# Kernel tuning notes

Measured on AMD Instinct MI355X. Metric: run time of the kernel, lower is better.

The kernel has to match this reference:

```python
import jax, jax.numpy as jnp
import numpy as np

N, E, DIM, L, NPERM, B = 20000, 640000, 128, 4, 20000, 256
R = NPERM * L * L  # rows of perm matrices
EPS = 1e-5


def _mlp(x, w1, b1, g, beta, w2, b2):
    # Linear -> BatchNorm (training-mode batch stats) -> ReLU -> Linear
    h = x @ w1 + b1
    mu = h.mean(0)
    var = h.var(0)  # biased, matches torch BN normalization
    h = (h - mu) * jax.lax.rsqrt(var + EPS) * g + beta
    return jax.nn.relu(h) @ w2 + b2


def setup_inputs() -> dict:
    key = jax.random.key(0)
    ks = jax.random.split(key, 40)
    s = 0.05
    inp = {}
    inp["node_feat"] = jax.random.normal(ks[0], (N, DIM), jnp.float32)
    inp["edge_feat"] = jax.random.normal(ks[1], (E, DIM), jnp.float32)
    inp["src"] = jax.random.randint(ks[2], (E,), 0, N)
    inp["dst"] = jax.random.randint(ks[3], (E,), 0, N)
    inp["rev_flag"] = jax.random.randint(ks[4], (E,), 0, 2).astype(bool)
    # sparse node_to_perm / edge_to_perm: one nnz per row (row i implicit)
    inp["n2p_cols"] = jax.random.randint(ks[5], (R,), 0, N)
    inp["n2p_vals"] = jax.random.uniform(ks[6], (R,), jnp.float32)
    inp["e2p_cols"] = jax.random.randint(ks[7], (R,), 0, E)
    inp["e2p_vals"] = jax.random.uniform(ks[8], (R,), jnp.float32)
    # sparse pooling matrix: perm j -> graph pool_rows[j] with weight pool_vals[j]
    inp["pool_rows"] = jax.random.randint(ks[9], (NPERM,), 0, B)
    inp["pool_vals"] = jax.random.uniform(ks[10], (NPERM,), jnp.float32)
    for i, n in enumerate(["in_w", "out_w", "src_w", "dst_w", "nloop_w", "eloop_w"]):
        inp[n] = jax.random.normal(ks[11 + i], (DIM, DIM), jnp.float32) * s
    inp["lrp_w"] = jax.random.normal(ks[17], (DIM, DIM, L * L), jnp.float32) * s
    inp["nbias"] = jnp.zeros((DIM,), jnp.float32)
    inp["ebias"] = jnp.zeros((DIM,), jnp.float32)
    inp["lrp_bias"] = jnp.zeros((DIM,), jnp.float32)
    for p, k0 in (("n", 20), ("e", 26)):
        inp[p + "mlp_w1"] = jax.random.normal(ks[k0], (DIM, DIM), jnp.float32) * s
        inp[p + "mlp_b1"] = jnp.zeros((DIM,), jnp.float32)
        inp[p + "mlp_g"] = jnp.ones((DIM,), jnp.float32)
        inp[p + "mlp_beta"] = jnp.zeros((DIM,), jnp.float32)
        inp[p + "mlp_w2"] = jax.random.normal(ks[k0 + 1], (DIM, DIM), jnp.float32) * s
        inp[p + "mlp_b2"] = jnp.zeros((DIM,), jnp.float32)
    return inp


def reference(node_feat, edge_feat, src, dst, rev_flag, n2p_cols, n2p_vals,
              e2p_cols, e2p_vals, pool_rows, pool_vals,
              in_w, out_w, src_w, dst_w, nloop_w, eloop_w, lrp_w,
              nbias, ebias, lrp_bias,
              nmlp_w1, nmlp_b1, nmlp_g, nmlp_beta, nmlp_w2, nmlp_b2,
              emlp_w1, emlp_b1, emlp_g, emlp_beta, emlp_w2, emlp_b2):
    hs = node_feat[src]   # [E, d]
    hd = node_feat[dst]   # [E, d]
    r = rev_flag[:, None]
    # per-edge messages with reverse-edge masking
    edge_msg = jnp.where(r, hs @ dst_w - hd @ src_w, hd @ dst_w - hs @ src_w)
    node_msg = jnp.where(r, edge_feat @ out_w, -(edge_feat @ in_w))
    node_agg = jax.ops.segment_sum(node_msg, dst, num_segments=N)
    # node update
    nout = _mlp(node_feat @ nloop_w + node_agg + nbias,
                nmlp_w1, nmlp_b1, nmlp_g, nmlp_beta, nmlp_w2, nmlp_b2)
    # edge update: degree-scaled term uses out-degree of dst node
    out_deg = jax.ops.segment_sum(jnp.ones((E,), jnp.float32), src, num_segments=N)
    dlog = jnp.log2(1.0 + out_deg[dst])[:, None]
    add = 2.0 * (1.0 + dlog) * (edge_feat @ (src_w - dst_w))
    eout = _mlp(edge_feat @ eloop_w + add + edge_msg + ebias,
                emlp_w1, emlp_b1, emlp_g, emlp_beta, emlp_w2, emlp_b2)
    # sparse perm gathers + LRP einsum + sparse pooling scatter
    perm = n2p_vals[:, None] * nout[n2p_cols] + e2p_vals[:, None] * eout[e2p_cols]
    perm = perm.reshape(NPERM, L * L, DIM)
    lrp = jnp.einsum('dab,bca->dc', perm, lrp_w) + lrp_bias
    pooled = jax.ops.segment_sum(pool_vals[:, None] * lrp, pool_rows, num_segments=B)
    return pooled, eout
```

## Files before the change

kernel.cpp:

```cpp
#include <hip/hip_runtime.h>
#include <stdint.h>

constexpr int Nn     = 20000;
constexpr int Ee     = 640000;
constexpr int NPERMc = 20000;

using bf16x8 = __attribute__((ext_vector_type(8))) short;
using f32x4  = __attribute__((ext_vector_type(4))) float;
using s16x4  = __attribute__((ext_vector_type(4))) short;
using u16x8  = __attribute__((ext_vector_type(8))) unsigned short;

__device__ __forceinline__ short f2bf(float f) {
  union { float f; unsigned u; } v; v.f = f;
  unsigned r = v.u + 0x7FFFu + ((v.u >> 16) & 1u);
  return (short)(r >> 16);
}
__device__ __forceinline__ float bf2f(unsigned short s) {
  union { unsigned u; float f; } v; v.u = ((unsigned)s) << 16;
  return v.f;
}
__device__ __forceinline__ f32x4 MFMA(bf16x8 a, bf16x8 b, f32x4 c) {
  return __builtin_amdgcn_mfma_f32_16x16x32_bf16(a, b, c, 0, 0, 0);
}

__device__ __forceinline__ int fragIdx(int k, int n) {
  int t = n >> 4, kk = k >> 5;
  int l = ((k & 31) >> 3) * 16 + (n & 15);
  int j = k & 7;
  return ((t * 4 + kk) * 64 + l) * 8 + j;
}

__device__ __forceinline__ void stage16x128(const float* __restrict__ src, int row0, int M,
                                            int lane, short* lds) {
  #pragma unroll
  for (int it = 0; it < 8; ++it) {
    int u = it * 64 + lane;
    int r = u >> 5;
    int q = u & 31;
    int row = row0 + r;
    float4 v = make_float4(0.f, 0.f, 0.f, 0.f);
    if (row < M) v = ((const float4*)(src + (size_t)row * 128))[q];
    int k  = q * 4;
    int kk = k >> 5;
    int l2 = ((k & 31) >> 3) * 16 + r;
    int j  = k & 7;
    s16x4 s4 = { f2bf(v.x), f2bf(v.y), f2bf(v.z), f2bf(v.w) };
    *(s16x4*)(lds + (kk * 64 + l2) * 8 + j) = s4;
  }
}

__global__ __launch_bounds__(256) void kPrep(
    const float* __restrict__ in_w,  const float* __restrict__ out_w,
    const float* __restrict__ src_w, const float* __restrict__ dst_w,
    const float* __restrict__ nloop_w, const float* __restrict__ eloop_w,
    const float* __restrict__ lrp_w,
    const float* __restrict__ nbias, const float* __restrict__ ebias,
    const float* __restrict__ w1e, const float* __restrict__ b1e,
    const float* __restrict__ w1n, const float* __restrict__ b1n,
    const float* __restrict__ w2e, const float* __restrict__ w2n,
    short* __restrict__ WA, short* __restrict__ BQ, short* __restrict__ WN,
    short* __restrict__ W2E, short* __restrict__ W2N, short* __restrict__ WL,
    float* __restrict__ c0e, float* __restrict__ c0n) {
  __shared__ float Rl[16384];
  int tid = threadIdx.x;
  int blk = blockIdx.x;
  if (blk < 448) {
    int p = blk >> 6, sub = blk & 63;
    const float* La; const float* Lb = nullptr; const float* R; short* outp;
    float sOut = 1.f;
    switch (p) {
      case 0: La = eloop_w;             R = w1e; outp = WA;          break;
      case 1: La = src_w; Lb = dst_w;   R = w1e; outp = WA + 16384;  break;
      case 2: La = dst_w;               R = w1e; outp = BQ;          break;
      case 3: La = src_w;               R = w1e; outp = BQ + 16384;  break;
      case 4: La = nloop_w;             R = w1n; outp = WN;          break;
      case 5: La = out_w;               R = w1n; outp = WN + 16384;  break;
      default: La = in_w;               R = w1n; outp = WN + 32768; sOut = -1.f; break;
    }
    for (int i = tid; i < 16384; i += 256) Rl[i] = R[i];
    __syncthreads();
    int e = sub * 256 + tid;
    int k = e >> 7, n = e & 127;
    float acc = 0.f;
    bool hasLb = (Lb != nullptr);
    for (int j = 0; j < 128; ++j) {
      float l = La[k * 128 + j];
      if (hasLb) l -= Lb[k * 128 + j];
      acc += l * Rl[j * 128 + n];
    }
    outp[fragIdx(k, n)] = f2bf(acc * sOut);
  } else if (blk < 512) {
    int e = (blk - 448) * 256 + tid; int k = e >> 7, n = e & 127;
    W2E[fragIdx(k, n)] = f2bf(w2e[k * 128 + n]);
  } else if (blk < 576) {
    int e = (blk - 512) * 256 + tid; int k = e >> 7, n = e & 127;
    W2N[fragIdx(k, n)] = f2bf(w2n[k * 128 + n]);
  } else if (blk < 1600) {
    int q = blk - 576; int a = q >> 6;
    int e = (q & 63) * 256 + tid; int k = e >> 7, n = e & 127;
    WL[a * 16384 + fragIdx(k, n)] = f2bf(lrp_w[(k * 128 + n) * 16 + a]);
  } else {
    if (tid < 128) {
      float acc = 0.f;
      for (int k2 = 0; k2 < 128; ++k2) acc += ebias[k2] * w1e[k2 * 128 + tid];
      c0e[tid] = acc + b1e[tid];
    } else {
      int n = tid - 128; float acc = 0.f;
      for (int k2 = 0; k2 < 128; ++k2) acc += nbias[k2] * w1n[k2 * 128 + n];
      c0n[n] = acc + b1n[n];
    }
  }
}


__global__ __launch_bounds__(256) void kHist(
    const int* __restrict__ srcI, const int* __restrict__ dstI,
    int* __restrict__ cnt, float* __restrict__ deg) {
  int e = blockIdx.x * 256 + threadIdx.x;
  atomicAdd(&cnt[dstI[e]], 1);
  atomicAdd(&deg[srcI[e]], 1.0f);
}

__global__ __launch_bounds__(256) void kScan(const int* __restrict__ cnt,
                                             int* __restrict__ off,
                                             int* __restrict__ cur) {
  __shared__ int lc[Nn];
  __shared__ int ps[256];
  int tid = threadIdx.x;
  for (int i = tid; i < Nn; i += 256) lc[i] = cnt[i];
  __syncthreads();
  constexpr int CH = (Nn + 255) / 256;
  int base = tid * CH;
  int local = 0;
  for (int i = 0; i < CH; ++i) {
    int idx = base + i;
    if (idx < Nn) local += lc[idx];
  }
  ps[tid] = local;
  __syncthreads();
  for (int d = 1; d < 256; d <<= 1) {
    int t = (tid >= d) ? ps[tid - d] : 0;
    __syncthreads();
    if (tid >= d) ps[tid] += t;
    __syncthreads();
  }
  int run = ps[tid] - local;
  for (int i = 0; i < CH; ++i) {
    int idx = base + i;
    if (idx < Nn) { off[idx] = run; cur[idx] = run; run += lc[idx]; }
  }
}

__global__ __launch_bounds__(256) void kScatter(
    const int* __restrict__ dstI, const int* __restrict__ revI,
    int* __restrict__ cur, int* __restrict__ order) {
  int e = blockIdx.x * 256 + threadIdx.x;
  int pos = atomicAdd(&cur[dstI[e]], 1);
  order[pos] = revI[e] ? (e | (int)0x80000000) : e;
}

__global__ __launch_bounds__(256) void kAgg2(
    const float* __restrict__ ef, const int* __restrict__ off,
    const int* __restrict__ cnt, const int* __restrict__ order,
    float* __restrict__ aggR, float* __restrict__ aggN) {
  int w = threadIdx.x >> 6, lane = threadIdx.x & 63;
  int n = blockIdx.x * 4 + w;
  if (n >= Nn) return;
  int s0 = off[n], c = cnt[n];
  float2 aR = make_float2(0.f, 0.f), aN = make_float2(0.f, 0.f);
  int i = 0;
  for (; i + 1 < c; i += 2) {
    int oe0 = order[s0 + i];
    int oe1 = order[s0 + i + 1];
    int e0 = oe0 & 0x7fffffff;
    int e1 = oe1 & 0x7fffffff;
    float2 v0 = ((const float2*)(ef + (size_t)e0 * 128))[lane];
    float2 v1 = ((const float2*)(ef + (size_t)e1 * 128))[lane];
    if (oe0 < 0) { aR.x += v0.x; aR.y += v0.y; } else { aN.x += v0.x; aN.y += v0.y; }
    if (oe1 < 0) { aR.x += v1.x; aR.y += v1.y; } else { aN.x += v1.x; aN.y += v1.y; }
  }
  if (i < c) {
    int oe = order[s0 + i];
    int e = oe & 0x7fffffff;
    float2 v = ((const float2*)(ef + (size_t)e * 128))[lane];
    if (oe < 0) { aR.x += v.x; aR.y += v.y; } else { aN.x += v.x; aN.y += v.y; }
  }
  ((float2*)(aggR + (size_t)n * 128))[lane] = aR;
  ((float2*)(aggN + (size_t)n * 128))[lane] = aN;
}

__global__ __launch_bounds__(256, 2) void kQ(const float* __restrict__ nf,
                                             const short* __restrict__ BQ,
                                             float* __restrict__ Q, int M) {
  __shared__ __align__(16) short alds[4][2048];
  __shared__ __align__(16) short wbuf[8192];
  int tid = threadIdx.x, w = tid >> 6, lane = tid & 63;
  int row0 = blockIdx.x * 64 + w * 16;
  stage16x128(nf, row0, M, lane, alds[w]);
  f32x4 acc[16];
  #pragma unroll
  for (int t = 0; t < 16; ++t) acc[t] = (f32x4){0.f, 0.f, 0.f, 0.f};
  const int4* g4 = (const int4*)BQ;
  for (int kk = 0; kk < 4; ++kk) {
    __syncthreads();
    for (int c = tid; c < 1024; c += 256) {
      int t = c >> 6, l = c & 63;
      ((int4*)wbuf)[c] = g4[(t * 4 + kk) * 64 + l];
    }
    __syncthreads();
    bf16x8 a = *(const bf16x8*)(alds[w] + (kk * 64 + lane) * 8);
    #pragma unroll
    for (int t = 0; t < 16; ++t) {
      bf16x8 b = *(const bf16x8*)(wbuf + (t * 64 + lane) * 8);
      acc[t] = MFMA(a, b, acc[t]);
    }
  }
  int sub = lane >> 4, m = lane & 15;
  #pragma unroll
  for (int i = 0; i < 4; ++i) {
    int row = row0 + sub * 4 + i;
    if (row < M) {
      #pragma unroll
      for (int h = 0; h < 2; ++h) {
        float4 f0, f1;
        f0.x = acc[h * 8 + 0][i]; f0.y = acc[h * 8 + 1][i];
        f0.z = acc[h * 8 + 2][i]; f0.w = acc[h * 8 + 3][i];
        f1.x = acc[h * 8 + 4][i]; f1.y = acc[h * 8 + 5][i];
        f1.z = acc[h * 8 + 6][i]; f1.w = acc[h * 8 + 7][i];
        float4* dst = (float4*)(Q + (size_t)row * 256 + h * 128 + m * 8);
        dst[0] = f0; dst[1] = f1;
      }
    }
  }
}

__global__ __launch_bounds__(256, 2) void kN1(
    const float* __restrict__ nf, const float* __restrict__ aggR,
    const float* __restrict__ aggN, const short* __restrict__ WN,
    const float* __restrict__ c0n, short* __restrict__ hN,
    float* __restrict__ scratchN, int M) {
  __shared__ __align__(16) short alds[4][2048];
  __shared__ __align__(16) short wlds[16384];
  __shared__ float statsLDS[256];
  int tid = threadIdx.x, w = tid >> 6, lane = tid & 63;
  statsLDS[tid] = 0.f;
  int row0 = blockIdx.x * 64 + w * 16;
  f32x4 acc[8];
  #pragma unroll
  for (int t = 0; t < 8; ++t) acc[t] = (f32x4){0.f, 0.f, 0.f, 0.f};
  for (int s = 0; s < 3; ++s) {
    const float* src = (s == 0) ? nf : ((s == 1) ? aggR : aggN);
    __syncthreads();
    const int4* g4 = (const int4*)(WN + s * 16384);
    for (int c = tid; c < 2048; c += 256) ((int4*)wlds)[c] = g4[c];
    __syncthreads();
    stage16x128(src, row0, M, lane, alds[w]);
    for (int kk = 0; kk < 4; ++kk) {
      bf16x8 a = *(const bf16x8*)(alds[w] + (kk * 64 + lane) * 8);
      #pragma unroll
      for (int t = 0; t < 8; ++t) {
        bf16x8 b = *(const bf16x8*)(wlds + ((t * 4 + kk) * 64 + lane) * 8);
        acc[t] = MFMA(a, b, acc[t]);
      }
    }
  }
  int sub = lane >> 4;
  #pragma unroll
  for (int t = 0; t < 8; ++t) {
    int col = t * 16 + (lane & 15);
    float c0 = c0n[col];
    float ss = 0.f, sq = 0.f;
    #pragma unroll
    for (int i = 0; i < 4; ++i) {
      int row = row0 + sub * 4 + i;
      float h = acc[t][i] + c0;
      if (row < M) { hN[(size_t)row * 128 + col] = f2bf(h); ss += h; sq += h * h; }
    }
    ss += __shfl_xor(ss, 16, 64); sq += __shfl_xor(sq, 16, 64);
    ss += __shfl_xor(ss, 32, 64); sq += __shfl_xor(sq, 32, 64);
    if (lane < 16) { atomicAdd(&statsLDS[col], ss); atomicAdd(&statsLDS[128 + col], sq); }
  }
  __syncthreads();
  scratchN[(size_t)tid * gridDim.x + blockIdx.x] = statsLDS[tid];
}

__global__ __launch_bounds__(256, 3) void kD(
    const float* __restrict__ ef, const short* __restrict__ WA,
    const float* __restrict__ Q, const float* __restrict__ c0e,
    const int* __restrict__ srcI, const int* __restrict__ dstI,
    const int* __restrict__ revI, const float* __restrict__ deg,
    short* __restrict__ hE, float* __restrict__ scratchE) {
  __shared__ __align__(16) short alds[4][2048];
  __shared__ float statsLDS[256];
  int tid = threadIdx.x, w = tid >> 6, lane = tid & 63;
  int m = lane & 15, sub = lane >> 4;
  statsLDS[tid] = 0.f;
  __syncthreads();
  int row0 = blockIdx.x * 64 + w * 16;
  float scl[4]; int qa[4], qb[4];
  #pragma unroll
  for (int i = 0; i < 4; ++i) {
    int e = row0 + sub * 4 + i;
    int s_ = srcI[e], d_ = dstI[e], r_ = revI[e];
    scl[i] = 2.0f * (1.0f + log2f(1.0f + deg[d_]));
    int na = r_ ? s_ : d_;
    int nb = r_ ? d_ : s_;
    qa[i] = na * 256 + m * 8;
    qb[i] = nb * 256 + 128 + m * 8;
  }
  stage16x128(ef, row0, Ee, lane, alds[w]);
  f32x4 acc1[8], acc2[8];
  #pragma unroll
  for (int t = 0; t < 8; ++t) { acc1[t] = (f32x4){0,0,0,0}; acc2[t] = (f32x4){0,0,0,0}; }
  const bf16x8* WB = (const bf16x8*)WA;
  #pragma unroll
  for (int kk = 0; kk < 4; ++kk) {
    bf16x8 a = *(const bf16x8*)(alds[w] + (kk * 64 + lane) * 8);
    #pragma unroll
    for (int t = 0; t < 8; ++t) {
      bf16x8 b1 = WB[(t * 4 + kk) * 64 + lane];
      bf16x8 b2 = WB[2048 + (t * 4 + kk) * 64 + lane];
      acc1[t] = MFMA(a, b1, acc1[t]);
      acc2[t] = MFMA(a, b2, acc2[t]);
    }
  }
  float c0[8];
  #pragma unroll
  for (int t = 0; t < 8; ++t) c0[t] = c0e[t * 16 + m];
  float ss[8], sq[8];
  #pragma unroll
  for (int t = 0; t < 8; ++t) { ss[t] = 0.f; sq[t] = 0.f; }
  #pragma unroll
  for (int i = 0; i < 4; ++i) {
    int e = row0 + sub * 4 + i;
    float4 A0 = ((const float4*)(Q + qa[i]))[0];
    float4 A1 = ((const float4*)(Q + qa[i]))[1];
    float4 B0 = ((const float4*)(Q + qb[i]))[0];
    float4 B1 = ((const float4*)(Q + qb[i]))[1];
    float qv[8] = {A0.x - B0.x, A0.y - B0.y, A0.z - B0.z, A0.w - B0.w,
                   A1.x - B1.x, A1.y - B1.y, A1.z - B1.z, A1.w - B1.w};
    #pragma unroll
    for (int t = 0; t < 8; ++t) {
      float h = acc1[t][i] + scl[i] * acc2[t][i] + qv[t] + c0[t];
      hE[(size_t)e * 128 + t * 16 + m] = f2bf(h);
      ss[t] += h; sq[t] += h * h;
    }
  }
  #pragma unroll
  for (int t = 0; t < 8; ++t) {
    float a = ss[t], b = sq[t];
    a += __shfl_xor(a, 16, 64); b += __shfl_xor(b, 16, 64);
    a += __shfl_xor(a, 32, 64); b += __shfl_xor(b, 32, 64);
    if (lane < 16) {
      atomicAdd(&statsLDS[t * 16 + lane], a);
      atomicAdd(&statsLDS[128 + t * 16 + lane], b);
    }
  }
  __syncthreads();
  scratchE[(size_t)tid * gridDim.x + blockIdx.x] = statsLDS[tid];
}

__global__ __launch_bounds__(256) void kFin(const float* __restrict__ scratch, int NB,
                                            float M, const float* __restrict__ g,
                                            const float* __restrict__ beta,
                                            float* __restrict__ st) {
  __shared__ float red[256];
  __shared__ float red2[256];
  int c = blockIdx.x;
  int tid = threadIdx.x;
  float s = 0.f, q = 0.f;
  for (int i = tid; i < NB; i += 256) {
    s += scratch[(size_t)c * NB + i];
    q += scratch[(size_t)(128 + c) * NB + i];
  }
  red[tid] = s; red2[tid] = q;
  __syncthreads();
  for (int off = 128; off > 0; off >>= 1) {
    if (tid < off) { red[tid] += red[tid + off]; red2[tid] += red2[tid + off]; }
    __syncthreads();
  }
  if (tid == 0) {
    float mu  = red[0] / M;
    float var = red2[0] / M - mu * mu;
    float inv = rsqrtf(var + 1e-5f);
    float sc  = g[c] * inv;
    st[c] = sc;
    st[128 + c] = beta[c] - mu * sc;
  }
}

__global__ __launch_bounds__(256, 2) void kF(const short* __restrict__ h,
                                             const float* __restrict__ st,
                                             const short* __restrict__ w2f,
                                             const float* __restrict__ b2,
                                             float* __restrict__ outp, int M) {
  __shared__ __align__(16) short alds[4][2048];
  __shared__ __align__(16) short wlds[16384];
  int tid = threadIdx.x, w = tid >> 6, lane = tid & 63;
  for (int c = tid; c < 2048; c += 256) ((int4*)wlds)[c] = ((const int4*)w2f)[c];
  int row0 = blockIdx.x * 64 + w * 16;
  #pragma unroll
  for (int it = 0; it < 4; ++it) {
    int u = it * 64 + lane;
    int r = u >> 4;
    int c8 = (u & 15) * 8;
    int row = row0 + r;
    u16x8 hv = {0, 0, 0, 0, 0, 0, 0, 0};
    if (row < M) hv = *(const u16x8*)(h + (size_t)row * 128 + c8);
    bf16x8 ov;
    #pragma unroll
    for (int q = 0; q < 8; ++q) {
      float f = bf2f(hv[q]);
      float v = fmaxf(f * st[c8 + q] + st[128 + c8 + q], 0.f);
      ov[q] = f2bf(v);
    }
    int kk = c8 >> 5;
    int l2 = ((c8 & 31) >> 3) * 16 + r;
    *(bf16x8*)(alds[w] + (kk * 64 + l2) * 8) = ov;
  }
  __syncthreads();
  f32x4 acc[8];
  #pragma unroll
  for (int t = 0; t < 8; ++t) acc[t] = (f32x4){0.f, 0.f, 0.f, 0.f};
  for (int kk = 0; kk < 4; ++kk) {
    bf16x8 a = *(const bf16x8*)(alds[w] + (kk * 64 + lane) * 8);
    #pragma unroll
    for (int t = 0; t < 8; ++t) {
      bf16x8 b = *(const bf16x8*)(wlds + ((t * 4 + kk) * 64 + lane) * 8);
      acc[t] = MFMA(a, b, acc[t]);
    }
  }
  int sub = lane >> 4;
  #pragma unroll
  for (int t = 0; t < 8; ++t) {
    int col = t * 16 + (lane & 15);
    float bb = b2[col];
    #pragma unroll
    for (int i = 0; i < 4; ++i) {
      int row = row0 + sub * 4 + i;
      if (row < M) outp[(size_t)row * 128 + col] = acc[t][i] + bb;
    }
  }
}

__global__ __launch_bounds__(256, 2) void kLRP(
    const float* __restrict__ nout, const float* __restrict__ eoutp,
    const int* __restrict__ n2pc, const float* __restrict__ n2pv,
    const int* __restrict__ e2pc, const float* __restrict__ e2pv,
    const int* __restrict__ poolr, const float* __restrict__ poolv,
    const short* __restrict__ WL, const float* __restrict__ lrp_bias,
    float* __restrict__ pooled) {
  __shared__ __align__(16) short alds[4][2048];
  __shared__ __align__(16) short wlds[16384];
  int tid = threadIdx.x, w = tid >> 6, lane = tid & 63;
  int row0 = blockIdx.x * 64 + w * 16;
  f32x4 acc[8];
  #pragma unroll
  for (int t = 0; t < 8; ++t) acc[t] = (f32x4){0.f, 0.f, 0.f, 0.f};
  for (int a = 0; a < 16; ++a) {
    __syncthreads();
    const int4* g4 = (const int4*)(WL + a * 16384);
    for (int c = tid; c < 2048; c += 256) ((int4*)wlds)[c] = g4[c];
    __syncthreads();
    #pragma unroll
    for (int it = 0; it < 8; ++it) {
      int u = it * 64 + lane;
      int r = u >> 5;
      int q = u & 31;
      int d = row0 + r;
      float4 v = make_float4(0.f, 0.f, 0.f, 0.f);
      if (d < NPERMc) {
        int i = d * 16 + a;
        int nc = n2pc[i]; float nv = n2pv[i];
        int ec = e2pc[i]; float ev = e2pv[i];
        float4 nr = ((const float4*)(nout  + (size_t)nc * 128))[q];
        float4 er = ((const float4*)(eoutp + (size_t)ec * 128))[q];
        v.x = nv * nr.x + ev * er.x;
        v.y = nv * nr.y + ev * er.y;
        v.z = nv * nr.z + ev * er.z;
        v.w = nv * nr.w + ev * er.w;
      }
      int k  = q * 4;
      int kk = k >> 5;
      int l2 = ((k & 31) >> 3) * 16 + r;
      int j  = k & 7;
      s16x4 s4 = { f2bf(v.x), f2bf(v.y), f2bf(v.z), f2bf(v.w) };
      *(s16x4*)(alds[w] + (kk * 64 + l2) * 8 + j) = s4;
    }
    for (int kk = 0; kk < 4; ++kk) {
      bf16x8 aa = *(const bf16x8*)(alds[w] + (kk * 64 + lane) * 8);
      #pragma unroll
      for (int t = 0; t < 8; ++t) {
        bf16x8 b = *(const bf16x8*)(wlds + ((t * 4 + kk) * 64 + lane) * 8);
        acc[t] = MFMA(aa, b, acc[t]);
      }
    }
  }
  int sub = lane >> 4;
  #pragma unroll
  for (int t = 0; t < 8; ++t) {
    int col = t * 16 + (lane & 15);
    float lb = lrp_bias[col];
    #pragma unroll
    for (int i = 0; i < 4; ++i) {
      int d = row0 + sub * 4 + i;
      if (d < NPERMc) {
        float val = acc[t][i] + lb;
        atomicAdd(&pooled[poolr[d] * 128 + col], poolv[d] * val);
      }
    }
  }
}

extern "C" void kernel_launch(void* const* d_in, const int* in_sizes, int n_in,
                              void* d_out, int out_size, void* d_ws, size_t ws_size,
                              hipStream_t stream) {
  (void)in_sizes; (void)n_in; (void)out_size; (void)ws_size;
  const float* node_feat = (const float*)d_in[0];
  const float* edge_feat = (const float*)d_in[1];
  const int*   srcI      = (const int*)d_in[2];
  const int*   dstI      = (const int*)d_in[3];
  const int*   revI      = (const int*)d_in[4];
  const int*   n2pc      = (const int*)d_in[5];
  const float* n2pv      = (const float*)d_in[6];
  const int*   e2pc      = (const int*)d_in[7];
  const float* e2pv      = (const float*)d_in[8];
  const int*   poolr     = (const int*)d_in[9];
  const float* poolv     = (const float*)d_in[10];
  const float* in_w      = (const float*)d_in[11];
  const float* out_w     = (const float*)d_in[12];
  const float* src_w     = (const float*)d_in[13];
  const float* dst_w     = (const float*)d_in[14];
  const float* nloop_w   = (const float*)d_in[15];
  const float* eloop_w   = (const float*)d_in[16];
  const float* lrp_w     = (const float*)d_in[17];
  const float* nbias     = (const float*)d_in[18];
  const float* ebias     = (const float*)d_in[19];
  const float* lrp_bias  = (const float*)d_in[20];
  const float* nmlp_w1   = (const float*)d_in[21];
  const float* nmlp_b1   = (const float*)d_in[22];
  const float* nmlp_g    = (const float*)d_in[23];
  const float* nmlp_beta = (const float*)d_in[24];
  const float* nmlp_w2   = (const float*)d_in[25];
  const float* nmlp_b2   = (const float*)d_in[26];
  const float* emlp_w1   = (const float*)d_in[27];
  const float* emlp_b1   = (const float*)d_in[28];
  const float* emlp_g    = (const float*)d_in[29];
  const float* emlp_beta = (const float*)d_in[30];
  const float* emlp_w2   = (const float*)d_in[31];
  const float* emlp_b2   = (const float*)d_in[32];

  float* pooled = (float*)d_out;
  float* eoutp  = (float*)d_out + 32768;

  char* p = (char*)d_ws;
  auto alloc = [&](size_t b) { char* r = p; p += (b + 255) & ~(size_t)255; return r; };
  short* hE   = (short*)alloc((size_t)Ee * 128 * 2);
  float* Qm   = (float*)alloc((size_t)Nn * 256 * 4);
  float* aggR = (float*)alloc((size_t)Nn * 128 * 4);
  float* aggN = (float*)alloc((size_t)Nn * 128 * 4);
  short* hN   = (short*)alloc((size_t)Nn * 128 * 2);
  float* nout = (float*)alloc((size_t)Nn * 128 * 4);
  float* deg  = (float*)alloc((size_t)Nn * 4);
  float* scrE = (float*)alloc((size_t)256 * 10000 * 4);
  float* scrN = (float*)alloc((size_t)256 * 313 * 4);
  float* stE  = (float*)alloc(256 * 4);
  float* stN  = (float*)alloc(256 * 4);
  short* WA   = (short*)alloc(32768 * 2);
  short* BQ   = (short*)alloc(32768 * 2);
  short* WN   = (short*)alloc(49152 * 2);
  short* W2E  = (short*)alloc(16384 * 2);
  short* W2N  = (short*)alloc(16384 * 2);
  short* WL   = (short*)alloc((size_t)16 * 16384 * 2);
  float* c0e  = (float*)alloc(128 * 4);
  float* c0n  = (float*)alloc(128 * 4);
  int*   cnt  = (int*)alloc((size_t)Nn * 4);
  int*   offA = (int*)alloc((size_t)Nn * 4);
  int*   cur  = (int*)alloc((size_t)Nn * 4);
  int*   order= (int*)alloc((size_t)Ee * 4);

  hipMemsetAsync(deg,  0, (size_t)Nn * 4, stream);
  hipMemsetAsync(cnt,  0, (size_t)Nn * 4, stream);
  hipMemsetAsync(pooled, 0, (size_t)32768 * 4, stream);

  kPrep<<<1601, 256, 0, stream>>>(in_w, out_w, src_w, dst_w, nloop_w, eloop_w, lrp_w,
                                  nbias, ebias, emlp_w1, emlp_b1, nmlp_w1, nmlp_b1,
                                  emlp_w2, nmlp_w2, WA, BQ, WN, W2E, W2N, WL, c0e, c0n);
  kHist<<<Ee / 256, 256, 0, stream>>>(srcI, dstI, cnt, deg);
  kScan<<<1, 256, 0, stream>>>(cnt, offA, cur);
  kScatter<<<Ee / 256, 256, 0, stream>>>(dstI, revI, cur, order);
  kAgg2<<<Nn / 4, 256, 0, stream>>>(edge_feat, offA, cnt, order, aggR, aggN);
  kQ<<<313, 256, 0, stream>>>(node_feat, BQ, Qm, Nn);
  kN1<<<313, 256, 0, stream>>>(node_feat, aggR, aggN, WN, c0n, hN, scrN, Nn);
  kD<<<10000, 256, 0, stream>>>(edge_feat, WA, Qm, c0e, srcI, dstI, revI, deg, hE, scrE);
  kFin<<<128, 256, 0, stream>>>(scrE, 10000, (float)Ee, emlp_g, emlp_beta, stE);
  kFin<<<128, 256, 0, stream>>>(scrN, 313, (float)Nn, nmlp_g, nmlp_beta, stN);
  kF<<<10000, 256, 0, stream>>>(hE, stE, W2E, emlp_b2, eoutp, Ee);
  kF<<<313, 256, 0, stream>>>(hN, stN, W2N, nmlp_b2, nout, Nn);
  kLRP<<<313, 256, 0, stream>>>(nout, eoutp, n2pc, n2pv, e2pc, e2pv,
                                poolr, poolv, WL, lrp_bias, pooled);
}
```

Measured before the change: 1.497 ms.

## Swizzle LDS A-tiles, double kD rows per wave with LDS-staged weights, pack bf16 stores

Adds an XOR swizzle to the LDS A-fragment layout in every GEMM kernel to cut bank conflicts. kD now handles 128 edges per block (32 per wave), stages weights in LDS per k-slice and reuses each B fragment for two A tiles, which halves the grid and the stats scratch. hN/hE outputs are written as packed 8-wide bf16 vectors instead of scalar stores, and kF's staging is reorganised to match the new fragment layout. The cost is more registers and LDS in kD (occupancy hint lowered from 3 to 2) plus extra barriers for the weight staging.

```diff
diff --git a/kernel.cpp b/kernel.cpp
--- a/kernel.cpp
+++ b/kernel.cpp
@@ -22,6 +22,8 @@
 __device__ __forceinline__ f32x4 MFMA(bf16x8 a, bf16x8 b, f32x4 c) {
   return __builtin_amdgcn_mfma_f32_16x16x32_bf16(a, b, c, 0, 0, 0);
 }
+
+__device__ __forceinline__ int swz(int s) { return s ^ (((s >> 7) & 7) << 3); }
 
 __device__ __forceinline__ int fragIdx(int k, int n) {
   int t = n >> 4, kk = k >> 5;
@@ -45,7 +47,7 @@
     int l2 = ((k & 31) >> 3) * 16 + r;
     int j  = k & 7;
     s16x4 s4 = { f2bf(v.x), f2bf(v.y), f2bf(v.z), f2bf(v.w) };
-    *(s16x4*)(lds + (kk * 64 + l2) * 8 + j) = s4;
+    *(s16x4*)(lds + swz((kk * 64 + l2) * 8 + j)) = s4;
   }
 }
 
@@ -208,7 +210,7 @@
       ((int4*)wbuf)[c] = g4[(t * 4 + kk) * 64 + l];
     }
     __syncthreads();
-    bf16x8 a = *(const bf16x8*)(alds[w] + (kk * 64 + lane) * 8);
+    bf16x8 a = *(const bf16x8*)(alds[w] + swz((kk * 64 + lane) * 8));
     #pragma unroll
     for (int t = 0; t < 16; ++t) {
       bf16x8 b = *(const bf16x8*)(wbuf + (t * 64 + lane) * 8);
@@ -243,6 +245,7 @@
   __shared__ __align__(16) short wlds[16384];
   __shared__ float statsLDS[256];
   int tid = threadIdx.x, w = tid >> 6, lane = tid & 63;
+  int m = lane & 15, sub = lane >> 4;
   statsLDS[tid] = 0.f;
   int row0 = blockIdx.x * 64 + w * 16;
   f32x4 acc[8];
@@ -256,7 +259,7 @@
     __syncthreads();
     stage16x128(src, row0, M, lane, alds[w]);
     for (int kk = 0; kk < 4; ++kk) {
-      bf16x8 a = *(const bf16x8*)(alds[w] + (kk * 64 + lane) * 8);
+      bf16x8 a = *(const bf16x8*)(alds[w] + swz((kk * 64 + lane) * 8));
       #pragma unroll
       for (int t = 0; t < 8; ++t) {
         bf16x8 b = *(const bf16x8*)(wlds + ((t * 4 + kk) * 64 + lane) * 8);
@@ -264,86 +267,119 @@
       }
     }
   }
-  int sub = lane >> 4;
+  float c0v[8];
+  #pragma unroll
+  for (int t = 0; t < 8; ++t) c0v[t] = c0n[t * 16 + m];
+  float ss[8], sq[8];
+  #pragma unroll
+  for (int t = 0; t < 8; ++t) { ss[t] = 0.f; sq[t] = 0.f; }
+  #pragma unroll
+  for (int i = 0; i < 4; ++i) {
+    int row = row0 + sub * 4 + i;
+    if (row < M) {
+      bf16x8 pk;
+      #pragma unroll
+      for (int t = 0; t < 8; ++t) {
+        float h = acc[t][i] + c0v[t];
+        pk[t] = f2bf(h); ss[t] += h; sq[t] += h * h;
+      }
+      *(bf16x8*)(hN + (size_t)row * 128 + m * 8) = pk;
+    }
+  }
   #pragma unroll
   for (int t = 0; t < 8; ++t) {
-    int col = t * 16 + (lane & 15);
-    float c0 = c0n[col];
-    float ss = 0.f, sq = 0.f;
-    #pragma unroll
-    for (int i = 0; i < 4; ++i) {
-      int row = row0 + sub * 4 + i;
-      float h = acc[t][i] + c0;
-      if (row < M) { hN[(size_t)row * 128 + col] = f2bf(h); ss += h; sq += h * h; }
-    }
-    ss += __shfl_xor(ss, 16, 64); sq += __shfl_xor(sq, 16, 64);
-    ss += __shfl_xor(ss, 32, 64); sq += __shfl_xor(sq, 32, 64);
-    if (lane < 16) { atomicAdd(&statsLDS[col], ss); atomicAdd(&statsLDS[128 + col], sq); }
+    float a = ss[t], b = sq[t];
+    a += __shfl_xor(a, 16, 64); b += __shfl_xor(b, 16, 64);
+    a += __shfl_xor(a, 32, 64); b += __shfl_xor(b, 32, 64);
+    if (lane < 16) {
+      atomicAdd(&statsLDS[t * 16 + lane], a);
+      atomicAdd(&statsLDS[128 + t * 16 + lane], b);
+    }
   }
   __syncthreads();
   scratchN[(size_t)tid * gridDim.x + blockIdx.x] = statsLDS[tid];
 }
 
-__global__ __launch_bounds__(256, 3) void kD(
+__global__ __launch_bounds__(256, 2) void kD(
     const float* __restrict__ ef, const short* __restrict__ WA,
     const float* __restrict__ Q, const float* __restrict__ c0e,
     const int* __restrict__ srcI, const int* __restrict__ dstI,
     const int* __restrict__ revI, const float* __restrict__ deg,
     short* __restrict__ hE, float* __restrict__ scratchE) {
-  __shared__ __align__(16) short alds[4][2048];
+  __shared__ __align__(16) short alds[4][4096];
+  __shared__ __align__(16) short wbuf[8192];
   __shared__ float statsLDS[256];
   int tid = threadIdx.x, w = tid >> 6, lane = tid & 63;
   int m = lane & 15, sub = lane >> 4;
   statsLDS[tid] = 0.f;
-  __syncthreads();
-  int row0 = blockIdx.x * 64 + w * 16;
-  float scl[4]; int qa[4], qb[4];
-  #pragma unroll
-  for (int i = 0; i < 4; ++i) {
-    int e = row0 + sub * 4 + i;
-    int s_ = srcI[e], d_ = dstI[e], r_ = revI[e];
-    scl[i] = 2.0f * (1.0f + log2f(1.0f + deg[d_]));
-    int na = r_ ? s_ : d_;
-    int nb = r_ ? d_ : s_;
-    qa[i] = na * 256 + m * 8;
-    qb[i] = nb * 256 + 128 + m * 8;
-  }
-  stage16x128(ef, row0, Ee, lane, alds[w]);
-  f32x4 acc1[8], acc2[8];
-  #pragma unroll
-  for (int t = 0; t < 8; ++t) { acc1[t] = (f32x4){0,0,0,0}; acc2[t] = (f32x4){0,0,0,0}; }
-  const bf16x8* WB = (const bf16x8*)WA;
-  #pragma unroll
+  int row0 = blockIdx.x * 128 + w * 32;
+  float scl[8]; int qa[8], qb[8];
+  #pragma unroll
+  for (int g = 0; g < 2; ++g)
+    #pragma unroll
+    for (int i = 0; i < 4; ++i) {
+      int e = row0 + g * 16 + sub * 4 + i;
+      int s_ = srcI[e], d_ = dstI[e], r_ = revI[e];
+      int x = g * 4 + i;
+      scl[x] = 2.0f * (1.0f + log2f(1.0f + deg[d_]));
+      int na = r_ ? s_ : d_;
+      int nb = r_ ? d_ : s_;
+      qa[x] = na * 256 + m * 8;
+      qb[x] = nb * 256 + 128 + m * 8;
+    }
+  stage16x128(ef, row0,      Ee, lane, alds[w]);
+  stage16x128(ef, row0 + 16, Ee, lane, alds[w] + 2048);
+  f32x4 acc1[2][8], acc2[2][8];
+  #pragma unroll
+  for (int g = 0; g < 2; ++g)
+    #pragma unroll
+    for (int t = 0; t < 8; ++t) { acc1[g][t] = (f32x4){0,0,0,0}; acc2[g][t] = (f32x4){0,0,0,0}; }
+  const int4* g4 = (const int4*)WA;
   for (int kk = 0; kk < 4; ++kk) {
-    bf16x8 a = *(const bf16x8*)(alds[w] + (kk * 64 + lane) * 8);
+    __syncthreads();
+    for (int c = tid; c < 1024; c += 256) {
+      int mm = c >> 9, t = (c >> 6) & 7, l = c & 63;
+      ((int4*)wbuf)[c] = g4[mm * 2048 + (t * 4 + kk) * 64 + l];
+    }
+    __syncthreads();
+    bf16x8 a0 = *(const bf16x8*)(alds[w] + swz((kk * 64 + lane) * 8));
+    bf16x8 a1 = *(const bf16x8*)(alds[w] + 2048 + swz((kk * 64 + lane) * 8));
     #pragma unroll
     for (int t = 0; t < 8; ++t) {
-      bf16x8 b1 = WB[(t * 4 + kk) * 64 + lane];
-      bf16x8 b2 = WB[2048 + (t * 4 + kk) * 64 + lane];
-      acc1[t] = MFMA(a, b1, acc1[t]);
-      acc2[t] = MFMA(a, b2, acc2[t]);
-    }
-  }
-  float c0[8];
-  #pragma unroll
-  for (int t = 0; t < 8; ++t) c0[t] = c0e[t * 16 + m];
+      bf16x8 b1 = *(const bf16x8*)(wbuf + (t * 64 + lane) * 8);
+      bf16x8 b2 = *(const bf16x8*)(wbuf + 4096 + (t * 64 + lane) * 8);
+      acc1[0][t] = MFMA(a0, b1, acc1[0][t]);
+      acc1[1][t] = MFMA(a1, b1, acc1[1][t]);
+      acc2[0][t] = MFMA(a0, b2, acc2[0][t]);
+      acc2[1][t] = MFMA(a1, b2, acc2[1][t]);
+    }
+  }
+  float c0v[8];
+  #pragma unroll
+  for (int t = 0; t < 8; ++t) c0v[t] = c0e[t * 16 + m];
   float ss[8], sq[8];
   #pragma unroll
   for (int t = 0; t < 8; ++t) { ss[t] = 0.f; sq[t] = 0.f; }
   #pragma unroll
-  for (int i = 0; i < 4; ++i) {
-    int e = row0 + sub * 4 + i;
-    float4 A0 = ((const float4*)(Q + qa[i]))[0];
-    float4 A1 = ((const float4*)(Q + qa[i]))[1];
-    float4 B0 = ((const float4*)(Q + qb[i]))[0];
-    float4 B1 = ((const float4*)(Q + qb[i]))[1];
-    float qv[8] = {A0.x - B0.x, A0.y - B0.y, A0.z - B0.z, A0.w - B0.w,
-                   A1.x - B1.x, A1.y - B1.y, A1.z - B1.z, A1.w - B1.w};
-    #pragma unroll
-    for (int t = 0; t < 8; ++t) {
-      float h = acc1[t][i] + scl[i] * acc2[t][i] + qv[t] + c0[t];
-      hE[(size_t)e * 128 + t * 16 + m] = f2bf(h);
-      ss[t] += h; sq[t] += h * h;
+  for (int g = 0; g < 2; ++g) {
+    #pragma unroll
+    for (int i = 0; i < 4; ++i) {
+      int x = g * 4 + i;
+      int e = row0 + g * 16 + sub * 4 + i;
+      float4 A0 = ((const float4*)(Q + qa[x]))[0];
+      float4 A1 = ((const float4*)(Q + qa[x]))[1];
+      float4 B0 = ((const float4*)(Q + qb[x]))[0];
+      float4 B1 = ((const float4*)(Q + qb[x]))[1];
+      float qv[8] = {A0.x - B0.x, A0.y - B0.y, A0.z - B0.z, A0.w - B0.w,
+                     A1.x - B1.x, A1.y - B1.y, A1.z - B1.z, A1.w - B1.w};
+      bf16x8 pk;
+      #pragma unroll
+      for (int t = 0; t < 8; ++t) {
+        float h = acc1[g][t][i] + scl[x] * acc2[g][t][i] + qv[t] + c0v[t];
+        pk[t] = f2bf(h);
+        ss[t] += h; sq[t] += h * h;
+      }
+      *(bf16x8*)(hE + (size_t)e * 128 + m * 8) = pk;
     }
   }
   #pragma unroll
@@ -397,33 +433,36 @@
   __shared__ __align__(16) short alds[4][2048];
   __shared__ __align__(16) short wlds[16384];
   int tid = threadIdx.x, w = tid >> 6, lane = tid & 63;
+  int m2 = lane & 15;
   for (int c = tid; c < 2048; c += 256) ((int4*)wlds)[c] = ((const int4*)w2f)[c];
   int row0 = blockIdx.x * 64 + w * 16;
+  float sc8[8], tb8[8];
+  #pragma unroll
+  for (int q = 0; q < 8; ++q) {
+    int col = q * 16 + m2;
+    sc8[q] = st[col]; tb8[q] = st[128 + col];
+  }
   #pragma unroll
   for (int it = 0; it < 4; ++it) {
-    int u = it * 64 + lane;
-    int r = u >> 4;
-    int c8 = (u & 15) * 8;
+    int r = it * 4 + (lane >> 4);
     int row = row0 + r;
     u16x8 hv = {0, 0, 0, 0, 0, 0, 0, 0};
-    if (row < M) hv = *(const u16x8*)(h + (size_t)row * 128 + c8);
-    bf16x8 ov;
+    if (row < M) hv = *(const u16x8*)(h + (size_t)row * 128 + m2 * 8);
     #pragma unroll
     for (int q = 0; q < 8; ++q) {
       float f = bf2f(hv[q]);
-      float v = fmaxf(f * st[c8 + q] + st[128 + c8 + q], 0.f);
-      ov[q] = f2bf(v);
-    }
-    int kk = c8 >> 5;
-    int l2 = ((c8 & 31) >> 3) * 16 + r;
-    *(bf16x8*)(alds[w] + (kk * 64 + l2) * 8) = ov;
+      float v = fmaxf(f * sc8[q] + tb8[q], 0.f);
+      int k = q * 16 + m2;
+      int kk = k >> 5, l2 = ((k & 31) >> 3) * 16 + r, j = k & 7;
+      alds[w][swz((kk * 64 + l2) * 8 + j)] = f2bf(v);
+    }
   }
   __syncthreads();
   f32x4 acc[8];
   #pragma unroll
   for (int t = 0; t < 8; ++t) acc[t] = (f32x4){0.f, 0.f, 0.f, 0.f};
   for (int kk = 0; kk < 4; ++kk) {
-    bf16x8 a = *(const bf16x8*)(alds[w] + (kk * 64 + lane) * 8);
+    bf16x8 a = *(const bf16x8*)(alds[w] + swz((kk * 64 + lane) * 8));
     #pragma unroll
     for (int t = 0; t < 8; ++t) {
       bf16x8 b = *(const bf16x8*)(wlds + ((t * 4 + kk) * 64 + lane) * 8);
@@ -485,10 +524,10 @@
       int l2 = ((k & 31) >> 3) * 16 + r;
       int j  = k & 7;
       s16x4 s4 = { f2bf(v.x), f2bf(v.y), f2bf(v.z), f2bf(v.w) };
-      *(s16x4*)(alds[w] + (kk * 64 + l2) * 8 + j) = s4;
+      *(s16x4*)(alds[w] + swz((kk * 64 + l2) * 8 + j)) = s4;
     }
     for (int kk = 0; kk < 4; ++kk) {
-      bf16x8 aa = *(const bf16x8*)(alds[w] + (kk * 64 + lane) * 8);
+      bf16x8 aa = *(const bf16x8*)(alds[w] + swz((kk * 64 + lane) * 8));
       #pragma unroll
       for (int t = 0; t < 8; ++t) {
         bf16x8 b = *(const bf16x8*)(wlds + ((t * 4 + kk) * 64 + lane) * 8);
@@ -562,7 +601,7 @@
   short* hN   = (short*)alloc((size_t)Nn * 128 * 2);
   float* nout = (float*)alloc((size_t)Nn * 128 * 4);
   float* deg  = (float*)alloc((size_t)Nn * 4);
-  float* scrE = (float*)alloc((size_t)256 * 10000 * 4);
+  float* scrE = (float*)alloc((size_t)256 * 5000 * 4);
   float* scrN = (float*)alloc((size_t)256 * 313 * 4);
   float* stE  = (float*)alloc(256 * 4);
   float* stN  = (float*)alloc(256 * 4);
@@ -592,8 +631,8 @@
   kAgg2<<<Nn / 4, 256, 0, stream>>>(edge_feat, offA, cnt, order, aggR, aggN);
   kQ<<<313, 256, 0, stream>>>(node_feat, BQ, Qm, Nn);
   kN1<<<313, 256, 0, stream>>>(node_feat, aggR, aggN, WN, c0n, hN, scrN, Nn);
-  kD<<<10000, 256, 0, stream>>>(edge_feat, WA, Qm, c0e, srcI, dstI, revI, deg, hE, scrE);
-  kFin<<<128, 256, 0, stream>>>(scrE, 10000, (float)Ee, emlp_g, emlp_beta, stE);
+  kD<<<5000, 256, 0, stream>>>(edge_feat, WA, Qm, c0e, srcI, dstI, revI, deg, hE, scrE);
+  kFin<<<128, 256, 0, stream>>>(scrE, 5000, (float)Ee, emlp_g, emlp_beta, stE);
   kFin<<<128, 256, 0, stream>>>(scrN, 313, (float)Nn, nmlp_g, nmlp_beta, stN);
   kF<<<10000, 256, 0, stream>>>(hE, stE, W2E, emlp_b2, eoutp, Ee);
   kF<<<313, 256, 0, stream>>>(hN, stN, W2N, nmlp_b2, nout, Nn);
```

New measurement: 1.419 ms. 5.2% less time.
